# Performance work log

Hardware: AMD Instinct MI355X
Metric: run time of the kernel (lower is better)

Reference implementation:

```python
import jax, jax.numpy as jnp
import numpy as np
from jax import lax

BITS = 8
CLIP = 2.0 ** (BITS - 1) - 1.0  # 127 for int8 symmetric quantization
EPS = 1e-6


def _quantize(x):
    """Dynamic per-tensor symmetric quantization (AQT-style).

    Returns the integer-valued (but float-dtype) quantized tensor and the
    scale such that dequant = q / scale.
    """
    bound = jnp.maximum(jnp.max(jnp.abs(x)), EPS)
    scale = CLIP / bound
    q = jnp.clip(jnp.round(x * scale), -CLIP, CLIP)
    return q, scale


def setup_inputs() -> dict:
    key = jax.random.key(0)
    k1, k2 = jax.random.split(key)
    lhs = jax.random.normal(k1, (4096, 4096), dtype=jnp.float32)
    rhs = jax.random.normal(k2, (4096, 4096), dtype=jnp.float32)
    return {"lhs": lhs, "rhs": rhs}


def reference(lhs, rhs):
    # Quantize both operands with dynamically computed per-tensor scales,
    # do the matmul on the integer-valued tensors, then dequantize the
    # result by the product of scales. This is the math aqt_ops.aqt_dot
    q_lhs, s_lhs = _quantize(lhs)
    q_rhs, s_rhs = _quantize(rhs)
    acc = jnp.matmul(q_lhs, q_rhs)  # [M, N], integer-valued accumulation
    return acc / (s_lhs * s_rhs)
```

## Files before the change

kernel.cpp:

```cpp
#include <hip/hip_runtime.h>
#include <hip/hip_bf16.h>


typedef int v4i __attribute__((ext_vector_type(4)));
typedef int v16i __attribute__((ext_vector_type(16)));

#define MAT_N 4096

__device__ __forceinline__ void async_copy16(const void* g, void* l) {
    __builtin_amdgcn_global_load_lds(
        (const __attribute__((address_space(1))) void*)g,
        (__attribute__((address_space(3))) void*)l,
        16, 0, 0);
}

__device__ __forceinline__ unsigned uabs_bits(float f) {
    return __float_as_uint(f) & 0x7fffffffu;
}

__global__ __launch_bounds__(256) void absmax_partial_kernel(
    const float4* __restrict__ lhs, const float4* __restrict__ rhs,
    unsigned* __restrict__ pmax) {
    const int b = blockIdx.x;
    const float4* x = (b < 512) ? lhs : rhs;
    const float4* p = x + (size_t)(b & 511) * 8192;
    unsigned m0 = 0, m1 = 0, m2 = 0, m3 = 0;
#pragma unroll 8
    for (int u = 0; u < 32; u++) {
        float4 v = p[u * 256 + threadIdx.x];
        m0 = max(m0, uabs_bits(v.x));
        m1 = max(m1, uabs_bits(v.y));
        m2 = max(m2, uabs_bits(v.z));
        m3 = max(m3, uabs_bits(v.w));
    }
    unsigned m = max(max(m0, m1), max(m2, m3));
#pragma unroll
    for (int off = 32; off > 0; off >>= 1)
        m = max(m, (unsigned)__shfl_down(m, off, 64));
    __shared__ unsigned sm[4];
    if ((threadIdx.x & 63) == 0) sm[threadIdx.x >> 6] = m;
    __syncthreads();
    if (threadIdx.x == 0)
        pmax[b] = max(max(sm[0], sm[1]), max(sm[2], sm[3]));
}

__global__ __launch_bounds__(256) void quant_fused_kernel(
    const float* __restrict__ lhs, const float* __restrict__ rhs,
    unsigned char* __restrict__ qA, signed char* __restrict__ qBT,
    const unsigned* __restrict__ pmax) {
    const int N = MAT_N;
    const int t = threadIdx.x;
    int b = blockIdx.x;
    __shared__ __align__(16) signed char smT[64 * 256];
    __shared__ unsigned red[4];
    __shared__ float s_sh;

    const int slot0 = (b < 4096) ? 0 : 512;
    unsigned mm = max(pmax[slot0 + t], pmax[slot0 + 256 + t]);
#pragma unroll
    for (int off = 32; off > 0; off >>= 1)
        mm = max(mm, (unsigned)__shfl_down(mm, off, 64));
    if ((t & 63) == 0) red[t >> 6] = mm;
    __syncthreads();
    if (t == 0) {
        unsigned f = max(max(red[0], red[1]), max(red[2], red[3]));
        s_sh = 127.0f / fmaxf(__uint_as_float(f), 1e-6f);
    }
    __syncthreads();
    const float s = s_sh;

    if (b < 4096) {
        const float4* x4 = (const float4*)lhs;
        unsigned* q4 = (unsigned*)qA;
        const int base4 = b * 1024;
#pragma unroll
        for (int u = 0; u < 4; u++) {
            int idx = base4 + u * 256 + t;
            float4 v = x4[idx];
            int a = min(127, max(-127, (int)rintf(v.x * s)));
            int bq = min(127, max(-127, (int)rintf(v.y * s)));
            int c = min(127, max(-127, (int)rintf(v.z * s)));
            int d = min(127, max(-127, (int)rintf(v.w * s)));
            q4[idx] = (unsigned)(a & 0xff) | ((unsigned)(bq & 0xff) << 8) |
                      ((unsigned)(c & 0xff) << 16) | ((unsigned)(d & 0xff) << 24);
        }
    } else {
        const int rb = b - 4096;
        const int n0 = (rb & 63) * 64;
        const int k0 = (rb >> 6) * 256;
        const int mk = t >> 4;
        const int mn = t & 15;
        const float4* x4 = (const float4*)rhs;

        float4 v[4][4];
#pragma unroll
        for (int ss = 0; ss < 4; ss++)
#pragma unroll
            for (int i = 0; i < 4; i++)
                v[ss][i] = x4[(size_t)(k0 + 64 * ss + 4 * mk + i) * (N / 4) +
                              (n0 >> 2) + mn];

        unsigned w[4][4];
#pragma unroll
        for (int ss = 0; ss < 4; ss++)
#pragma unroll
            for (int i = 0; i < 4; i++) {
                int a = min(127, max(-127, (int)rintf(v[ss][i].x * s)));
                int bq = min(127, max(-127, (int)rintf(v[ss][i].y * s)));
                int c = min(127, max(-127, (int)rintf(v[ss][i].z * s)));
                int d = min(127, max(-127, (int)rintf(v[ss][i].w * s)));
                w[ss][i] =
                    (unsigned)(a & 0xff) | ((unsigned)(bq & 0xff) << 8) |
                    ((unsigned)(c & 0xff) << 16) | ((unsigned)(d & 0xff) << 24);
            }

#pragma unroll
        for (int ss = 0; ss < 4; ss++) {
            const int cq = 4 * ss + (mk >> 2);
            const int off = (mk & 3) * 4;
#pragma unroll
            for (int j = 0; j < 4; j++) {
                unsigned selj = (unsigned)j | ((unsigned)(4 + j) << 8) |
                                ((unsigned)j << 16) | ((unsigned)(4 + j) << 24);
                unsigned p01 = __builtin_amdgcn_perm(w[ss][1], w[ss][0], selj);
                unsigned p23 = __builtin_amdgcn_perm(w[ss][3], w[ss][2], selj);
                unsigned uj = __builtin_amdgcn_perm(p23, p01, 0x05040100u);
                const int nr = 4 * mn + j;
                *(unsigned*)(smT + nr * 256 + ((cq ^ (nr & 15)) << 4) + off) = uj;
            }
        }
        __syncthreads();

#pragma unroll
        for (int wq = 0; wq < 4; wq++) {
            const int idx = wq * 256 + t;
            const int nr = idx >> 4;
            const int cl = idx & 15;
            int4 val = *(const int4*)(smT + nr * 256 + ((cl ^ (nr & 15)) << 4));
            *(int4*)(qBT + (size_t)(n0 + nr) * N + k0 + cl * 16) = val;
        }
    }
}

#define MFMA_I8 __builtin_amdgcn_mfma_i32_32x32x32_i8
#define SBAR0() __builtin_amdgcn_sched_barrier(0)
#define BARRIER() __builtin_amdgcn_s_barrier()

__global__ __launch_bounds__(512, 2) void gemm_i8_kernel(
    const signed char* __restrict__ A, const signed char* __restrict__ BT,
    float* __restrict__ C, const unsigned* __restrict__ pmax) {
    const int N = MAT_N;
    __shared__ __align__(16) signed char As[2][256 * 128];
    __shared__ __align__(16) signed char Bs[2][256 * 128];
    __shared__ unsigned redl[8], redr[8];

    const int tid = threadIdx.x;
    const int wave = tid >> 6;
    const int lane = tid & 63;
    const int m32 = lane & 31;
    const int h = lane >> 5;
    const int wm = wave >> 2;
    const int wn = wave & 3;

    const int bid = blockIdx.x;
    const int xcd = bid & 7;
    const int bi = bid >> 3;
    const int by = (xcd >> 1) * 4 + (bi >> 3);
    const int bx = (xcd & 1) * 8 + (bi & 7);
    const int brow = by * 256;
    const int bcol = bx * 256;

    v16i acc[4][2] = {};

    int gaoff[4], gboff[4], lofs[4];
#pragma unroll
    for (int u = 0; u < 4; u++) {
        int c = tid + 512 * u;
        int r = c >> 3;
        int q = (c & 7) ^ ((r ^ (r >> 3)) & 7);
        gaoff[u] = (brow + r) * N + q * 16;
        gboff[u] = (bcol + r) * N + q * 16;
        lofs[u] = c * 16;
    }

    int arow[4], av[4];
#pragma unroll
    for (int mi = 0; mi < 4; mi++) {
        int r = wm * 128 + mi * 32 + m32;
        arow[mi] = r * 128;
        av[mi] = (r ^ (r >> 3)) & 7;
    }
    int bro[2], bv[2];
#pragma unroll
    for (int nj = 0; nj < 2; nj++) {
        int r = wn * 64 + nj * 32 + m32;
        bro[nj] = r * 128;
        bv[nj] = (r ^ (r >> 3)) & 7;
    }

#pragma unroll
    for (int u = 0; u < 4; u++) async_copy16(A + gaoff[u], &As[0][lofs[u]]);
#pragma unroll
    for (int u = 0; u < 4; u++) async_copy16(BT + gboff[u], &Bs[0][lofs[u]]);
    asm volatile("s_waitcnt vmcnt(0)" ::: "memory");
    BARRIER();
    SBAR0();

    for (int t = 0; t < 32; ++t) {
        const signed char* as_ = As[t & 1];
        const signed char* bs_ = Bs[t & 1];
        signed char* na = As[(t & 1) ^ 1];
        signed char* nb = Bs[(t & 1) ^ 1];
        const int nko = (t + 1) * 128;
        const bool st = (t < 31);

#define LDA_(mi, s) (*(const v4i*)(as_ + arow[mi] + (((2 * (s) + h) ^ av[mi]) << 4)))
#define LDB_(nj, s) (*(const v4i*)(bs_ + bro[nj] + (((2 * (s) + h) ^ bv[nj]) << 4)))

        v4i bf00, bf01, bf10, bf11;

        {
            v4i a00 = LDA_(0, 0), a01 = LDA_(0, 1);
            v4i a10 = LDA_(1, 0), a11 = LDA_(1, 1);
            bf00 = LDB_(0, 0); bf01 = LDB_(0, 1);
            bf10 = LDB_(1, 0); bf11 = LDB_(1, 1);
            if (st) {
#pragma unroll
                for (int u = 0; u < 4; u++)
                    async_copy16(A + gaoff[u] + nko, na + lofs[u]);
            }
            SBAR0();
            BARRIER();
            asm volatile("s_waitcnt lgkmcnt(0)" ::: "memory");
            SBAR0();
            __builtin_amdgcn_s_setprio(1);
            acc[0][0] = MFMA_I8(a00, bf00, acc[0][0], 0, 0, 0);
            acc[0][1] = MFMA_I8(a00, bf10, acc[0][1], 0, 0, 0);
            acc[1][0] = MFMA_I8(a10, bf00, acc[1][0], 0, 0, 0);
            acc[1][1] = MFMA_I8(a10, bf10, acc[1][1], 0, 0, 0);
            acc[0][0] = MFMA_I8(a01, bf01, acc[0][0], 0, 0, 0);
            acc[0][1] = MFMA_I8(a01, bf11, acc[0][1], 0, 0, 0);
            acc[1][0] = MFMA_I8(a11, bf01, acc[1][0], 0, 0, 0);
            acc[1][1] = MFMA_I8(a11, bf11, acc[1][1], 0, 0, 0);
            __builtin_amdgcn_s_setprio(0);
            BARRIER();
        }
        {
            v4i a20 = LDA_(2, 0), a21 = LDA_(2, 1);
            v4i a30 = LDA_(3, 0), a31 = LDA_(3, 1);
            if (st) {
#pragma unroll
                for (int u = 0; u < 4; u++)
                    async_copy16(BT + gboff[u] + nko, nb + lofs[u]);
            }
            SBAR0();
            BARRIER();
            asm volatile("s_waitcnt lgkmcnt(0)" ::: "memory");
            SBAR0();
            __builtin_amdgcn_s_setprio(1);
            acc[2][0] = MFMA_I8(a20, bf00, acc[2][0], 0, 0, 0);
            acc[2][1] = MFMA_I8(a20, bf10, acc[2][1], 0, 0, 0);
            acc[3][0] = MFMA_I8(a30, bf00, acc[3][0], 0, 0, 0);
            acc[3][1] = MFMA_I8(a30, bf10, acc[3][1], 0, 0, 0);
            acc[2][0] = MFMA_I8(a21, bf01, acc[2][0], 0, 0, 0);
            acc[2][1] = MFMA_I8(a21, bf11, acc[2][1], 0, 0, 0);
            acc[3][0] = MFMA_I8(a31, bf01, acc[3][0], 0, 0, 0);
            acc[3][1] = MFMA_I8(a31, bf11, acc[3][1], 0, 0, 0);
            __builtin_amdgcn_s_setprio(0);
            BARRIER();
        }
        {
            v4i a00 = LDA_(0, 2), a01 = LDA_(0, 3);
            v4i a10 = LDA_(1, 2), a11 = LDA_(1, 3);
            bf00 = LDB_(0, 2); bf01 = LDB_(0, 3);
            bf10 = LDB_(1, 2); bf11 = LDB_(1, 3);
            SBAR0();
            BARRIER();
            asm volatile("s_waitcnt lgkmcnt(0)" ::: "memory");
            SBAR0();
            __builtin_amdgcn_s_setprio(1);
            acc[0][0] = MFMA_I8(a00, bf00, acc[0][0], 0, 0, 0);
            acc[0][1] = MFMA_I8(a00, bf10, acc[0][1], 0, 0, 0);
            acc[1][0] = MFMA_I8(a10, bf00, acc[1][0], 0, 0, 0);
            acc[1][1] = MFMA_I8(a10, bf10, acc[1][1], 0, 0, 0);
            acc[0][0] = MFMA_I8(a01, bf01, acc[0][0], 0, 0, 0);
            acc[0][1] = MFMA_I8(a01, bf11, acc[0][1], 0, 0, 0);
            acc[1][0] = MFMA_I8(a11, bf01, acc[1][0], 0, 0, 0);
            acc[1][1] = MFMA_I8(a11, bf11, acc[1][1], 0, 0, 0);
            __builtin_amdgcn_s_setprio(0);
            BARRIER();
        }
        {
            v4i a20 = LDA_(2, 2), a21 = LDA_(2, 3);
            v4i a30 = LDA_(3, 2), a31 = LDA_(3, 3);
            SBAR0();
            BARRIER();
            asm volatile("s_waitcnt lgkmcnt(0)" ::: "memory");
            SBAR0();
            __builtin_amdgcn_s_setprio(1);
            acc[2][0] = MFMA_I8(a20, bf00, acc[2][0], 0, 0, 0);
            acc[2][1] = MFMA_I8(a20, bf10, acc[2][1], 0, 0, 0);
            acc[3][0] = MFMA_I8(a30, bf00, acc[3][0], 0, 0, 0);
            acc[3][1] = MFMA_I8(a30, bf10, acc[3][1], 0, 0, 0);
            acc[2][0] = MFMA_I8(a21, bf01, acc[2][0], 0, 0, 0);
            acc[2][1] = MFMA_I8(a21, bf11, acc[2][1], 0, 0, 0);
            acc[3][0] = MFMA_I8(a31, bf01, acc[3][0], 0, 0, 0);
            acc[3][1] = MFMA_I8(a31, bf11, acc[3][1], 0, 0, 0);
            __builtin_amdgcn_s_setprio(0);
            if (st) {
                asm volatile("s_waitcnt vmcnt(0)" ::: "memory");
            }
            BARRIER();
            SBAR0();
        }
#undef LDA_
#undef LDB_
    }

    unsigned ml = pmax[tid];
    unsigned mr = pmax[512 + tid];
#pragma unroll
    for (int off = 32; off > 0; off >>= 1) {
        ml = max(ml, (unsigned)__shfl_down(ml, off, 64));
        mr = max(mr, (unsigned)__shfl_down(mr, off, 64));
    }
    if (lane == 0) { redl[wave] = ml; redr[wave] = mr; }
    __syncthreads();
    unsigned fl = redl[0], fr = redr[0];
#pragma unroll
    for (int k = 1; k < 8; k++) {
        fl = max(fl, redl[k]);
        fr = max(fr, redr[k]);
    }
    const float bl = fmaxf(__uint_as_float(fl), 1e-6f);
    const float br = fmaxf(__uint_as_float(fr), 1e-6f);
    const float dq = bl * br * (1.0f / (127.0f * 127.0f));

#pragma unroll
    for (int mi = 0; mi < 4; mi++)
#pragma unroll
        for (int nj = 0; nj < 2; nj++) {
            const int col = bcol + wn * 64 + nj * 32 + m32;
#pragma unroll
            for (int reg = 0; reg < 16; reg++) {
                const int row =
                    brow + wm * 128 + mi * 32 + (reg & 3) + 8 * (reg >> 2) + 4 * h;
                C[(size_t)row * N + col] = (float)acc[mi][nj][reg] * dq;
            }
        }
}

extern "C" void kernel_launch(void* const* d_in, const int* in_sizes, int n_in,
                              void* d_out, int out_size, void* d_ws, size_t ws_size,
                              hipStream_t stream) {
    const float* lhs = (const float*)d_in[0];
    const float* rhs = (const float*)d_in[1];
    float* out = (float*)d_out;

    unsigned* pmax = (unsigned*)d_ws;
    signed char* qA = (signed char*)d_ws + 8192;
    signed char* qBT = qA + (size_t)MAT_N * MAT_N;

    absmax_partial_kernel<<<1024, 256, 0, stream>>>(
        (const float4*)lhs, (const float4*)rhs, pmax);
    quant_fused_kernel<<<5120, 256, 0, stream>>>(
        lhs, rhs, (unsigned char*)qA, qBT, pmax);
    gemm_i8_kernel<<<256, 512, 0, stream>>>(qA, qBT, out, pmax);
}
```

Measured before the change: 262.5 us.

## Pre-swizzle B into MFMA fragment layout and load it directly to registers

The quantize kernel now writes B in a blocked layout matching the MFMA operand fragments, so the GEMM can load B fragments straight from global memory into registers with register double-buffering. B's LDS staging is removed, which halves LDS use and cuts barriers from four to two per K-tile. The trade is that each wave re-fetches its B fragments from global or L2 with no LDS sharing across the waves that need them, adding memory traffic and latency exposure. The absmax kernel is also launched twice, which looks accidental and adds redundant work.

```diff
diff --git a/kernel.cpp b/kernel.cpp
--- a/kernel.cpp
+++ b/kernel.cpp
@@ -46,7 +46,7 @@
 
 __global__ __launch_bounds__(256) void quant_fused_kernel(
     const float* __restrict__ lhs, const float* __restrict__ rhs,
-    unsigned char* __restrict__ qA, signed char* __restrict__ qBT,
+    unsigned char* __restrict__ qA, signed char* __restrict__ qB2,
     const unsigned* __restrict__ pmax) {
     const int N = MAT_N;
     const int t = threadIdx.x;
@@ -134,10 +134,13 @@
 #pragma unroll
         for (int wq = 0; wq < 4; wq++) {
             const int idx = wq * 256 + t;
-            const int nr = idx >> 4;
-            const int cl = idx & 15;
-            int4 val = *(const int4*)(smT + nr * 256 + ((cl ^ (nr & 15)) << 4));
-            *(int4*)(qBT + (size_t)(n0 + nr) * N + k0 + cl * 16) = val;
+            const int row = idx & 31;
+            const int ql = (idx >> 5) & 15;
+            const int nb = idx >> 9;
+            const int nr = nb * 32 + row;
+            int4 val = *(const int4*)(smT + nr * 256 + ((ql ^ (nr & 15)) << 4));
+            *(int4*)(qB2 + (size_t)((n0 >> 5) + nb) * 131072 +
+                     (size_t)((k0 >> 4) + ql) * 512 + row * 16) = val;
         }
     }
 }
@@ -147,11 +150,10 @@
 #define BARRIER() __builtin_amdgcn_s_barrier()
 
 __global__ __launch_bounds__(512, 2) void gemm_i8_kernel(
-    const signed char* __restrict__ A, const signed char* __restrict__ BT,
+    const signed char* __restrict__ A, const signed char* __restrict__ B2,
     float* __restrict__ C, const unsigned* __restrict__ pmax) {
     const int N = MAT_N;
     __shared__ __align__(16) signed char As[2][256 * 128];
-    __shared__ __align__(16) signed char Bs[2][256 * 128];
     __shared__ unsigned redl[8], redr[8];
 
     const int tid = threadIdx.x;
@@ -172,14 +174,13 @@
 
     v16i acc[4][2] = {};
 
-    int gaoff[4], gboff[4], lofs[4];
+    int gaoff[4], lofs[4];
 #pragma unroll
     for (int u = 0; u < 4; u++) {
         int c = tid + 512 * u;
         int r = c >> 3;
         int q = (c & 7) ^ ((r ^ (r >> 3)) & 7);
         gaoff[u] = (brow + r) * N + q * 16;
-        gboff[u] = (bcol + r) * N + q * 16;
         lofs[u] = c * 16;
     }
 
@@ -190,131 +191,90 @@
         arow[mi] = r * 128;
         av[mi] = (r ^ (r >> 3)) & 7;
     }
-    int bro[2], bv[2];
-#pragma unroll
-    for (int nj = 0; nj < 2; nj++) {
-        int r = wn * 64 + nj * 32 + m32;
-        bro[nj] = r * 128;
-        bv[nj] = (r ^ (r >> 3)) & 7;
-    }
+    size_t b2b[2];
+#pragma unroll
+    for (int nj = 0; nj < 2; nj++)
+        b2b[nj] = (size_t)((bcol + wn * 64 + nj * 32) >> 5) * 131072 +
+                  m32 * 16 + h * 512;
+
+    v4i bA_[2][4], bB_[2][4];
 
 #pragma unroll
     for (int u = 0; u < 4; u++) async_copy16(A + gaoff[u], &As[0][lofs[u]]);
 #pragma unroll
-    for (int u = 0; u < 4; u++) async_copy16(BT + gboff[u], &Bs[0][lofs[u]]);
+    for (int nj = 0; nj < 2; nj++)
+#pragma unroll
+        for (int s = 0; s < 4; s++)
+            bA_[nj][s] = *(const v4i*)(B2 + b2b[nj] + s * 1024);
     asm volatile("s_waitcnt vmcnt(0)" ::: "memory");
     BARRIER();
     SBAR0();
 
-    for (int t = 0; t < 32; ++t) {
+    auto tile_body = [&](int t, v4i (&bC)[2][4], v4i (&bN)[2][4], bool ldn) {
         const signed char* as_ = As[t & 1];
-        const signed char* bs_ = Bs[t & 1];
         signed char* na = As[(t & 1) ^ 1];
-        signed char* nb = Bs[(t & 1) ^ 1];
-        const int nko = (t + 1) * 128;
-        const bool st = (t < 31);
-
-#define LDA_(mi, s) (*(const v4i*)(as_ + arow[mi] + (((2 * (s) + h) ^ av[mi]) << 4)))
-#define LDB_(nj, s) (*(const v4i*)(bs_ + bro[nj] + (((2 * (s) + h) ^ bv[nj]) << 4)))
-
-        v4i bf00, bf01, bf10, bf11;
-
+        if (ldn) {
+#pragma unroll
+            for (int u = 0; u < 4; u++)
+                async_copy16(A + gaoff[u] + (t + 1) * 128, na + lofs[u]);
+#pragma unroll
+            for (int nj = 0; nj < 2; nj++)
+#pragma unroll
+                for (int s = 0; s < 4; s++)
+                    bN[nj][s] = *(const v4i*)(B2 + b2b[nj] +
+                                              (size_t)(t + 1) * 4096 + s * 1024);
+        }
         {
-            v4i a00 = LDA_(0, 0), a01 = LDA_(0, 1);
-            v4i a10 = LDA_(1, 0), a11 = LDA_(1, 1);
-            bf00 = LDB_(0, 0); bf01 = LDB_(0, 1);
-            bf10 = LDB_(1, 0); bf11 = LDB_(1, 1);
-            if (st) {
-#pragma unroll
-                for (int u = 0; u < 4; u++)
-                    async_copy16(A + gaoff[u] + nko, na + lofs[u]);
-            }
-            SBAR0();
-            BARRIER();
+            v4i a[4][2];
+#pragma unroll
+            for (int mi = 0; mi < 4; mi++)
+#pragma unroll
+                for (int s = 0; s < 2; s++)
+                    a[mi][s] = *(const v4i*)(as_ + arow[mi] +
+                                             (((2 * s + h) ^ av[mi]) << 4));
             asm volatile("s_waitcnt lgkmcnt(0)" ::: "memory");
             SBAR0();
             __builtin_amdgcn_s_setprio(1);
-            acc[0][0] = MFMA_I8(a00, bf00, acc[0][0], 0, 0, 0);
-            acc[0][1] = MFMA_I8(a00, bf10, acc[0][1], 0, 0, 0);
-            acc[1][0] = MFMA_I8(a10, bf00, acc[1][0], 0, 0, 0);
-            acc[1][1] = MFMA_I8(a10, bf10, acc[1][1], 0, 0, 0);
-            acc[0][0] = MFMA_I8(a01, bf01, acc[0][0], 0, 0, 0);
-            acc[0][1] = MFMA_I8(a01, bf11, acc[0][1], 0, 0, 0);
-            acc[1][0] = MFMA_I8(a11, bf01, acc[1][0], 0, 0, 0);
-            acc[1][1] = MFMA_I8(a11, bf11, acc[1][1], 0, 0, 0);
+#pragma unroll
+            for (int s = 0; s < 2; s++)
+#pragma unroll
+                for (int mi = 0; mi < 4; mi++)
+#pragma unroll
+                    for (int nj = 0; nj < 2; nj++)
+                        acc[mi][nj] =
+                            MFMA_I8(a[mi][s], bC[nj][s], acc[mi][nj], 0, 0, 0);
             __builtin_amdgcn_s_setprio(0);
             BARRIER();
         }
         {
-            v4i a20 = LDA_(2, 0), a21 = LDA_(2, 1);
-            v4i a30 = LDA_(3, 0), a31 = LDA_(3, 1);
-            if (st) {
-#pragma unroll
-                for (int u = 0; u < 4; u++)
-                    async_copy16(BT + gboff[u] + nko, nb + lofs[u]);
-            }
-            SBAR0();
-            BARRIER();
+            v4i a[4][2];
+#pragma unroll
+            for (int mi = 0; mi < 4; mi++)
+#pragma unroll
+                for (int s = 0; s < 2; s++)
+                    a[mi][s] = *(const v4i*)(as_ + arow[mi] +
+                                             (((2 * (s + 2) + h) ^ av[mi]) << 4));
             asm volatile("s_waitcnt lgkmcnt(0)" ::: "memory");
             SBAR0();
             __builtin_amdgcn_s_setprio(1);
-            acc[2][0] = MFMA_I8(a20, bf00, acc[2][0], 0, 0, 0);
-            acc[2][1] = MFMA_I8(a20, bf10, acc[2][1], 0, 0, 0);
-            acc[3][0] = MFMA_I8(a30, bf00, acc[3][0], 0, 0, 0);
-            acc[3][1] = MFMA_I8(a30, bf10, acc[3][1], 0, 0, 0);
-            acc[2][0] = MFMA_I8(a21, bf01, acc[2][0], 0, 0, 0);
-            acc[2][1] = MFMA_I8(a21, bf11, acc[2][1], 0, 0, 0);
-            acc[3][0] = MFMA_I8(a31, bf01, acc[3][0], 0, 0, 0);
-            acc[3][1] = MFMA_I8(a31, bf11, acc[3][1], 0, 0, 0);
+#pragma unroll
+            for (int s = 0; s < 2; s++)
+#pragma unroll
+                for (int mi = 0; mi < 4; mi++)
+#pragma unroll
+                    for (int nj = 0; nj < 2; nj++)
+                        acc[mi][nj] = MFMA_I8(a[mi][s], bC[nj][s + 2],
+                                              acc[mi][nj], 0, 0, 0);
             __builtin_amdgcn_s_setprio(0);
-            BARRIER();
-        }
-        {
-            v4i a00 = LDA_(0, 2), a01 = LDA_(0, 3);
-            v4i a10 = LDA_(1, 2), a11 = LDA_(1, 3);
-            bf00 = LDB_(0, 2); bf01 = LDB_(0, 3);
-            bf10 = LDB_(1, 2); bf11 = LDB_(1, 3);
-            SBAR0();
-            BARRIER();
-            asm volatile("s_waitcnt lgkmcnt(0)" ::: "memory");
-            SBAR0();
-            __builtin_amdgcn_s_setprio(1);
-            acc[0][0] = MFMA_I8(a00, bf00, acc[0][0], 0, 0, 0);
-            acc[0][1] = MFMA_I8(a00, bf10, acc[0][1], 0, 0, 0);
-            acc[1][0] = MFMA_I8(a10, bf00, acc[1][0], 0, 0, 0);
-            acc[1][1] = MFMA_I8(a10, bf10, acc[1][1], 0, 0, 0);
-            acc[0][0] = MFMA_I8(a01, bf01, acc[0][0], 0, 0, 0);
-            acc[0][1] = MFMA_I8(a01, bf11, acc[0][1], 0, 0, 0);
-            acc[1][0] = MFMA_I8(a11, bf01, acc[1][0], 0, 0, 0);
-            acc[1][1] = MFMA_I8(a11, bf11, acc[1][1], 0, 0, 0);
-            __builtin_amdgcn_s_setprio(0);
-            BARRIER();
-        }
-        {
-            v4i a20 = LDA_(2, 2), a21 = LDA_(2, 3);
-            v4i a30 = LDA_(3, 2), a31 = LDA_(3, 3);
-            SBAR0();
-            BARRIER();
-            asm volatile("s_waitcnt lgkmcnt(0)" ::: "memory");
-            SBAR0();
-            __builtin_amdgcn_s_setprio(1);
-            acc[2][0] = MFMA_I8(a20, bf00, acc[2][0], 0, 0, 0);
-            acc[2][1] = MFMA_I8(a20, bf10, acc[2][1], 0, 0, 0);
-            acc[3][0] = MFMA_I8(a30, bf00, acc[3][0], 0, 0, 0);
-            acc[3][1] = MFMA_I8(a30, bf10, acc[3][1], 0, 0, 0);
-            acc[2][0] = MFMA_I8(a21, bf01, acc[2][0], 0, 0, 0);
-            acc[2][1] = MFMA_I8(a21, bf11, acc[2][1], 0, 0, 0);
-            acc[3][0] = MFMA_I8(a31, bf01, acc[3][0], 0, 0, 0);
-            acc[3][1] = MFMA_I8(a31, bf11, acc[3][1], 0, 0, 0);
-            __builtin_amdgcn_s_setprio(0);
-            if (st) {
-                asm volatile("s_waitcnt vmcnt(0)" ::: "memory");
-            }
+            asm volatile("s_waitcnt vmcnt(0)" ::: "memory");
             BARRIER();
             SBAR0();
         }
-#undef LDA_
-#undef LDB_
+    };
+
+    for (int tt = 0; tt < 16; ++tt) {
+        tile_body(2 * tt, bA_, bB_, true);
+        tile_body(2 * tt + 1, bB_, bA_, tt < 15);
     }
 
     unsigned ml = pmax[tid];
@@ -359,11 +319,13 @@
 
     unsigned* pmax = (unsigned*)d_ws;
     signed char* qA = (signed char*)d_ws + 8192;
-    signed char* qBT = qA + (size_t)MAT_N * MAT_N;
-
+    signed char* qB2 = qA + (size_t)MAT_N * MAT_N;
+
+    absmax_partial_kernel<<<1024, 256, 0, stream>>>(
+        (const float4*)lhs, (const float4*)rhs, pmax);
     absmax_partial_kernel<<<1024, 256, 0, stream>>>(
         (const float4*)lhs, (const float4*)rhs, pmax);
     quant_fused_kernel<<<5120, 256, 0, stream>>>(
-        lhs, rhs, (unsigned char*)qA, qBT, pmax);
-    gemm_i8_kernel<<<256, 512, 0, stream>>>(qA, qBT, out, pmax);
-}
+        lhs, rhs, (unsigned char*)qA, qB2, pmax);
+    gemm_i8_kernel<<<256, 512, 0, stream>>>(qA, qB2, out, pmax);
+}
```

Measured after the change: 288.6 us. 9.9% more time.

## Triple-buffer the A tile to prefetch two K-steps ahead

Applied to the files above, without the earlier changes.

Gives the A operand three LDS buffers so its global-to-LDS loads are issued two iterations ahead. The B buffer stays double-buffered. The end-of-iteration wait becomes vmcnt(4), which leaves the A(t+2) copies in flight. The aim is to hide more global-load latency behind the MFMA work. To keep LDS usage within the per-CU limit, the small reduction arrays for the scale computation now reuse the A buffer after the main loop, and the extra LDS use leaves no headroom for occupancy.

```diff
diff --git a/kernel.cpp b/kernel.cpp
--- a/kernel.cpp
+++ b/kernel.cpp
@@ -150,9 +150,8 @@
     const signed char* __restrict__ A, const signed char* __restrict__ BT,
     float* __restrict__ C, const unsigned* __restrict__ pmax) {
     const int N = MAT_N;
-    __shared__ __align__(16) signed char As[2][256 * 128];
+    __shared__ __align__(16) signed char As[3][256 * 128];
     __shared__ __align__(16) signed char Bs[2][256 * 128];
-    __shared__ unsigned redl[8], redr[8];
 
     const int tid = threadIdx.x;
     const int wave = tid >> 6;
@@ -202,17 +201,21 @@
     for (int u = 0; u < 4; u++) async_copy16(A + gaoff[u], &As[0][lofs[u]]);
 #pragma unroll
     for (int u = 0; u < 4; u++) async_copy16(BT + gboff[u], &Bs[0][lofs[u]]);
-    asm volatile("s_waitcnt vmcnt(0)" ::: "memory");
+#pragma unroll
+    for (int u = 0; u < 4; u++)
+        async_copy16(A + gaoff[u] + 128, &As[1][lofs[u]]);
+    asm volatile("s_waitcnt vmcnt(4)" ::: "memory");
     BARRIER();
     SBAR0();
 
     for (int t = 0; t < 32; ++t) {
-        const signed char* as_ = As[t & 1];
+        const int t3 = t % 3;
+        const signed char* as_ = As[t3];
         const signed char* bs_ = Bs[t & 1];
-        signed char* na = As[(t & 1) ^ 1];
+        signed char* na = As[(t + 2) % 3];
         signed char* nb = Bs[(t & 1) ^ 1];
-        const int nko = (t + 1) * 128;
-        const bool st = (t < 31);
+        const bool stB = (t < 31);
+        const bool stA = (t < 30);
 
 #define LDA_(mi, s) (*(const v4i*)(as_ + arow[mi] + (((2 * (s) + h) ^ av[mi]) << 4)))
 #define LDB_(nj, s) (*(const v4i*)(bs_ + bro[nj] + (((2 * (s) + h) ^ bv[nj]) << 4)))
@@ -224,10 +227,10 @@
             v4i a10 = LDA_(1, 0), a11 = LDA_(1, 1);
             bf00 = LDB_(0, 0); bf01 = LDB_(0, 1);
             bf10 = LDB_(1, 0); bf11 = LDB_(1, 1);
-            if (st) {
+            if (stB) {
 #pragma unroll
                 for (int u = 0; u < 4; u++)
-                    async_copy16(A + gaoff[u] + nko, na + lofs[u]);
+                    async_copy16(BT + gboff[u] + (t + 1) * 128, nb + lofs[u]);
             }
             SBAR0();
             BARRIER();
@@ -248,10 +251,10 @@
         {
             v4i a20 = LDA_(2, 0), a21 = LDA_(2, 1);
             v4i a30 = LDA_(3, 0), a31 = LDA_(3, 1);
-            if (st) {
+            if (stA) {
 #pragma unroll
                 for (int u = 0; u < 4; u++)
-                    async_copy16(BT + gboff[u] + nko, nb + lofs[u]);
+                    async_copy16(A + gaoff[u] + (t + 2) * 128, na + lofs[u]);
             }
             SBAR0();
             BARRIER();
@@ -307,7 +310,9 @@
             acc[3][0] = MFMA_I8(a31, bf01, acc[3][0], 0, 0, 0);
             acc[3][1] = MFMA_I8(a31, bf11, acc[3][1], 0, 0, 0);
             __builtin_amdgcn_s_setprio(0);
-            if (st) {
+            if (t < 30) {
+                asm volatile("s_waitcnt vmcnt(4)" ::: "memory");
+            } else if (t == 30) {
                 asm volatile("s_waitcnt vmcnt(0)" ::: "memory");
             }
             BARRIER();
@@ -317,6 +322,7 @@
 #undef LDB_
     }
 
+    unsigned* red = (unsigned*)&As[0][0];
     unsigned ml = pmax[tid];
     unsigned mr = pmax[512 + tid];
 #pragma unroll
@@ -324,13 +330,13 @@
         ml = max(ml, (unsigned)__shfl_down(ml, off, 64));
         mr = max(mr, (unsigned)__shfl_down(mr, off, 64));
     }
-    if (lane == 0) { redl[wave] = ml; redr[wave] = mr; }
+    if (lane == 0) { red[wave] = ml; red[8 + wave] = mr; }
     __syncthreads();
-    unsigned fl = redl[0], fr = redr[0];
+    unsigned fl = red[0], fr = red[8];
 #pragma unroll
     for (int k = 1; k < 8; k++) {
-        fl = max(fl, redl[k]);
-        fr = max(fr, redr[k]);
+        fl = max(fl, red[k]);
+        fr = max(fr, red[8 + k]);
     }
     const float bl = fmaxf(__uint_as_float(fl), 1e-6f);
     const float br = fmaxf(__uint_as_float(fr), 1e-6f);
```

Result: no change. 261.9 us (-0.2%).
